# Optimization experiments

Hardware: AMD Instinct MI355X
Metric: run time of the kernel (lower is better)

## Reference

```python
import jax, jax.numpy as jnp
import numpy as np

N = 100000   # nodes
E = 1000000  # edges
IN, H, OUT = 256, 64, 16


def setup_inputs() -> dict:
    key = jax.random.key(0)
    k0, k1, k2, k3 = jax.random.split(key, 4)
    x = jax.random.normal(k0, (N, IN), jnp.float32)
    edge_index = jax.random.randint(k1, (2, E), 0, N)
    # GCNConv parameters (glorot-ish weights, zero bias as in PyG defaults)
    W1 = jax.random.normal(k2, (IN, H), jnp.float32) / np.sqrt(IN).astype(np.float32)
    b1 = jnp.zeros((H,), jnp.float32)
    W2 = jax.random.normal(k3, (H, OUT), jnp.float32) / np.sqrt(H).astype(np.float32)
    b2 = jnp.zeros((OUT,), jnp.float32)
    return {"x": x, "edge_index": edge_index, "W1": W1, "b1": b1, "W2": W2, "b2": b2}


def gcn_conv(x, W, b, src, dst, n):
    # PyG GCNConv: h = x @ W; out[v] = sum_{(u->v)} norm(u,v) * h[u] + b
    h = x @ W                                    # [n, out]
    deg = jnp.zeros((n,), h.dtype).at[dst].add(1.0)
    dinv = jnp.where(deg > 0, jax.lax.rsqrt(deg), 0.0)
    norm = dinv[src] * dinv[dst]                 # [E+n] symmetric normalization
    msg = h[src] * norm[:, None]                 # gather + scale
    agg = jax.ops.segment_sum(msg, dst, num_segments=n)  # scatter-add
    return agg + b


def reference(x, edge_index, W1, b1, W2, b2):
    n = x.shape[0]
    # add self-loops (PyG GCNConv default add_self_loops=True)
    loops = jnp.arange(n, dtype=edge_index.dtype)
    src = jnp.concatenate([edge_index[0], loops])
    dst = jnp.concatenate([edge_index[1], loops])
    h = gcn_conv(x, W1, b1, src, dst, n)
    h = jax.nn.relu(h)  # F.dropout is identity in eval mode (training=False)
    return gcn_conv(h, W2, b2, src, dst, n)
```

## Files before the change

### kernel.cpp

```cpp
#include <hip/hip_runtime.h>

namespace {
constexpr int NN  = 100000;
constexpr int NE  = 1000000;
constexpr int INF = 256;
constexpr int HF  = 64;
constexpr int OF  = 16;
constexpr int SCAN_CHUNK = 1024;
constexpr int NBLK = (NN + SCAN_CHUNK - 1) / SCAN_CHUNK;
constexpr int NSEG = 8;
constexpr int SEGW = (NN + NSEG - 1) / NSEG;
constexpr int CNTW = 100096;
constexpr int ZBLK = (CNTW / 4 + 255) / 256;
constexpr int GB   = (NN + 127) / 128;
constexpr int ECHUNK = 2048;
constexpr int EGRP = (NE + ECHUNK - 1) / ECHUNK;
constexpr int SB   = EGRP * NSEG;
}

typedef __attribute__((ext_vector_type(8))) short     sh8;
typedef __attribute__((ext_vector_type(4))) float     f32x4;
typedef __attribute__((ext_vector_type(8))) unsigned short us8;

__device__ __forceinline__ unsigned short f2bf(float f) {
    unsigned int u = __builtin_bit_cast(unsigned int, f);
    u += 0x7FFFu + ((u >> 16) & 1u);
    return (unsigned short)(u >> 16);
}
__device__ __forceinline__ float bf2f(unsigned short s) {
    return __builtin_bit_cast(float, (unsigned int)s << 16);
}

__global__ void k_pre(int* __restrict__ cnt, const float* __restrict__ W1,
                      unsigned short* __restrict__ wt_g) {
    int b = blockIdx.x, t = threadIdx.x;
    if (b < ZBLK) {
        int i = (b * 256 + t) * 4;
        if (i < CNTW) *(int4*)(cnt + i) = (int4){0, 0, 0, 0};
    } else {
        int idx = (b - ZBLK) * 256 + t;
        int c = idx >> 8, k = idx & 255;
        wt_g[idx] = f2bf(W1[(size_t)k * HF + c]);
    }
}

__global__ __launch_bounds__(256) void k_hist(const int* __restrict__ dst,
                                              int* __restrict__ cnt) {
    int b   = blockIdx.x;
    int seg = b & (NSEG - 1);
    int grp = b >> 3;
    int e0  = grp * ECHUNK + threadIdx.x;
    int d[8];
    #pragma unroll
    for (int i = 0; i < 8; ++i) {
        int e = e0 + i * 256;
        d[i] = (e < NE) ? dst[e] : -1;
    }
    #pragma unroll
    for (int i = 0; i < 8; ++i) {
        if ((unsigned)d[i] / (unsigned)SEGW == (unsigned)seg)
            atomicAdd(&cnt[d[i]], 1);
    }
}

__global__ __launch_bounds__(256) void k_reduce(const int* __restrict__ cnt,
                                                int* __restrict__ bsum,
                                                float* __restrict__ dinv) {
    int t = threadIdx.x;
    int i0 = blockIdx.x * SCAN_CHUNK + t * 4;
    int s = 0;
    float dv[4] = {0.f, 0.f, 0.f, 0.f};
    #pragma unroll
    for (int q = 0; q < 4; ++q) {
        if (i0 + q < NN) {
            int c = cnt[i0 + q];
            s += c;
            dv[q] = rsqrtf((float)(c + 1));
        }
    }
    if (i0 + 3 < NN) *(float4*)(dinv + i0) = (float4){dv[0], dv[1], dv[2], dv[3]};
    else { for (int q = 0; q < 4; ++q) if (i0 + q < NN) dinv[i0 + q] = dv[q]; }
    #pragma unroll
    for (int off = 32; off > 0; off >>= 1) s += __shfl_down(s, off);
    __shared__ int wsum[4];
    int lane = t & 63, wid = t >> 6;
    if (lane == 0) wsum[wid] = s;
    __syncthreads();
    if (t == 0) bsum[blockIdx.x] = wsum[0] + wsum[1] + wsum[2] + wsum[3];
}

__global__ __launch_bounds__(256) void k_scan(const int* __restrict__ cnt,
                                              const int* __restrict__ bsum,
                                              int* __restrict__ rowptr,
                                              int* __restrict__ cursor) {
    int t = threadIdx.x;
    int b = blockIdx.x;
    int lane = t & 63, wid = t >> 6;

    int p = 0;
    if (lane < b) p += bsum[lane];
    if (64 + lane < b) p += bsum[64 + lane];
    #pragma unroll
    for (int off = 32; off > 0; off >>= 1) p += __shfl_down(p, off);
    int blockBase = __shfl(p, 0);

    int i0 = b * SCAN_CHUNK + t * 4;
    int v0 = 0, v1 = 0, v2 = 0, v3 = 0;
    if (i0 + 0 < NN) v0 = cnt[i0 + 0];
    if (i0 + 1 < NN) v1 = cnt[i0 + 1];
    if (i0 + 2 < NN) v2 = cnt[i0 + 2];
    if (i0 + 3 < NN) v3 = cnt[i0 + 3];
    int tsum = v0 + v1 + v2 + v3;
    int incl = tsum;
    #pragma unroll
    for (int off = 1; off < 64; off <<= 1) {
        int n = __shfl_up(incl, off);
        if (lane >= off) incl += n;
    }
    __shared__ int wsum[4];
    if (lane == 63) wsum[wid] = incl;
    __syncthreads();
    int woff = 0;
    for (int w = 0; w < wid; ++w) woff += wsum[w];
    int excl = woff + (incl - tsum) + blockBase;
    int e0 = excl, e1 = e0 + v0, e2 = e1 + v1, e3 = e2 + v2;
    if (i0 + 0 < NN) { rowptr[i0 + 0] = e0; cursor[i0 + 0] = e0; }
    if (i0 + 1 < NN) { rowptr[i0 + 1] = e1; cursor[i0 + 1] = e1; }
    if (i0 + 2 < NN) { rowptr[i0 + 2] = e2; cursor[i0 + 2] = e2; }
    if (i0 + 3 < NN) { rowptr[i0 + 3] = e3; cursor[i0 + 3] = e3; }
    if (i0 + 3 == NN - 1) rowptr[NN] = e3 + v3;
}

__global__ __launch_bounds__(256, 8) void k_gs(const float* __restrict__ x,
                                               const unsigned short* __restrict__ wt_g,
                                               unsigned short* __restrict__ h1,
                                               const int* __restrict__ src,
                                               const int* __restrict__ dst,
                                               int* __restrict__ cursor,
                                               int* __restrict__ eidx) {
    __shared__ unsigned short wt[64 * 136];
    int b = blockIdx.x;
    int t = threadIdx.x;

    if (b >= GB) {
        int sb  = b - GB;
        int seg = sb & (NSEG - 1);
        int grp = sb >> 3;
        int e0  = grp * ECHUNK + t;
        int d[8];
        #pragma unroll
        for (int i = 0; i < 8; ++i) {
            int e = e0 + i * 256;
            d[i] = (e < NE) ? dst[e] : -1;
        }
        #pragma unroll
        for (int i = 0; i < 8; ++i) {
            if ((unsigned)d[i] / (unsigned)SEGW == (unsigned)seg) {
                int p = atomicAdd(&cursor[d[i]], 1);
                eidx[p] = src[e0 + i * 256];
            }
        }
        return;
    }

    int w = t >> 6, l = t & 63;
    int row0 = b * 128;
    int m = l & 15;
    int g = l >> 4;
    int gr0 = row0 + w * 32 + m;      if (gr0 > NN - 1) gr0 = NN - 1;
    int gr1 = row0 + w * 32 + 16 + m; if (gr1 > NN - 1) gr1 = NN - 1;
    const float* p0 = x + (size_t)gr0 * INF + g * 8;
    const float* p1 = x + (size_t)gr1 * INF + g * 8;

    f32x4 acc[2][4];
    #pragma unroll
    for (int i = 0; i < 2; ++i)
        #pragma unroll
        for (int j = 0; j < 4; ++j) acc[i][j] = (f32x4){0.f, 0.f, 0.f, 0.f};

    #pragma unroll
    for (int half = 0; half < 2; ++half) {
        __syncthreads();
        #pragma unroll
        for (int p = 0; p < 4; ++p) {
            int T   = p * 256 + t;
            int c   = T >> 4;
            int kb8 = T & 15;
            *(us8*)(wt + c * 136 + kb8 * 8) =
                *(const us8*)(wt_g + c * 256 + half * 128 + kb8 * 8);
        }
        __syncthreads();

        #pragma unroll
        for (int kb = 0; kb < 128; kb += 32) {
            float4 u0 = *(const float4*)(p0 + half * 128 + kb);
            float4 u1 = *(const float4*)(p0 + half * 128 + kb + 4);
            float4 u2 = *(const float4*)(p1 + half * 128 + kb);
            float4 u3 = *(const float4*)(p1 + half * 128 + kb + 4);
            us8 a0u = { f2bf(u0.x), f2bf(u0.y), f2bf(u0.z), f2bf(u0.w),
                        f2bf(u1.x), f2bf(u1.y), f2bf(u1.z), f2bf(u1.w) };
            us8 a1u = { f2bf(u2.x), f2bf(u2.y), f2bf(u2.z), f2bf(u2.w),
                        f2bf(u3.x), f2bf(u3.y), f2bf(u3.z), f2bf(u3.w) };
            sh8 a0 = __builtin_bit_cast(sh8, a0u);
            sh8 a1 = __builtin_bit_cast(sh8, a1u);
            #pragma unroll
            for (int nt = 0; nt < 4; ++nt) {
                sh8 bb = *(const sh8*)(wt + (nt * 16 + m) * 136 + kb + g * 8);
                acc[0][nt] = __builtin_amdgcn_mfma_f32_16x16x32_bf16(a0, bb, acc[0][nt], 0, 0, 0);
                acc[1][nt] = __builtin_amdgcn_mfma_f32_16x16x32_bf16(a1, bb, acc[1][nt], 0, 0, 0);
            }
        }
    }

    #pragma unroll
    for (int mt = 0; mt < 2; ++mt) {
        #pragma unroll
        for (int r = 0; r < 4; ++r) {
            int gr = row0 + w * 32 + mt * 16 + (l >> 4) * 4 + r;
            if (gr < NN) {
                #pragma unroll
                for (int nt = 0; nt < 4; ++nt)
                    h1[(size_t)gr * HF + nt * 16 + (l & 15)] = f2bf(acc[mt][nt][r]);
            }
        }
    }
}

__global__ __launch_bounds__(256) void k_gather1(const int* __restrict__ rowptr,
                                                 const int* __restrict__ eidx,
                                                 const float* __restrict__ dinv,
                                                 const unsigned short* __restrict__ h1,
                                                 const float* __restrict__ b1,
                                                 const float* __restrict__ W2,
                                                 unsigned short* __restrict__ h2) {
    __shared__ float w2L[HF * OF];
    __shared__ float hrL[32][HF + 4];
    int t = threadIdx.x;
    *(float4*)(w2L + t * 4) = *(const float4*)(W2 + t * 4);

    int nodeL = t >> 3;
    int fg    = t & 7;
    int v     = blockIdx.x * 32 + nodeL;
    int beg = rowptr[v], end = rowptr[v + 1];

    float acc[8] = {};
    int   s_n = 0;  float w_n = 0.f;  us8 h_n = {};
    if (beg < end) {
        s_n = eidx[beg];
        w_n = dinv[s_n];
        h_n = *(const us8*)(h1 + (size_t)s_n * HF + fg * 8);
    }
    for (int i = beg; i < end; ++i) {
        float w_c = w_n;  us8 h_c = h_n;
        if (i + 1 < end) {
            s_n = eidx[i + 1];
            w_n = dinv[s_n];
            h_n = *(const us8*)(h1 + (size_t)s_n * HF + fg * 8);
        }
        #pragma unroll
        for (int q = 0; q < 8; ++q) acc[q] += w_c * bf2f(h_c[q]);
    }

    {
        float dv = dinv[v], sl = dv * dv;
        us8 hv = *(const us8*)(h1 + (size_t)v * HF + fg * 8);
        #pragma unroll
        for (int q = 0; q < 8; ++q) {
            float val = dv * acc[q] + sl * bf2f(hv[q]) + b1[fg * 8 + q];
            hrL[nodeL][fg * 8 + q] = val > 0.f ? val : 0.f;
        }
    }
    __syncthreads();

    #pragma unroll
    for (int T = t; T < 512; T += 256) {
        int n = T >> 4, j = T & 15;
        const float* hr = hrL[n];
        float p = 0.f;
        #pragma unroll
        for (int k = 0; k < HF; ++k) p += hr[k] * w2L[k * OF + j];
        h2[(size_t)(blockIdx.x * 32 + n) * OF + j] = f2bf(p);
    }
}

__global__ __launch_bounds__(256) void k_gather2(const int* __restrict__ rowptr,
                                                 const int* __restrict__ eidx,
                                                 const float* __restrict__ dinv,
                                                 const unsigned short* __restrict__ h2,
                                                 const float* __restrict__ b2,
                                                 float* __restrict__ out) {
    int t     = threadIdx.x;
    int nodeL = t >> 4;
    int j     = t & 15;
    int v     = blockIdx.x * 16 + nodeL;
    int beg = rowptr[v], end = rowptr[v + 1];

    float acc = 0.f;
    int   s_n = 0;  float w_n = 0.f;  unsigned short h_n = 0;
    if (beg < end) {
        s_n = eidx[beg];
        w_n = dinv[s_n];
        h_n = h2[(size_t)s_n * OF + j];
    }
    for (int i = beg; i < end; ++i) {
        float w_c = w_n;  unsigned short h_c = h_n;
        if (i + 1 < end) {
            s_n = eidx[i + 1];
            w_n = dinv[s_n];
            h_n = h2[(size_t)s_n * OF + j];
        }
        acc += w_c * bf2f(h_c);
    }
    float dv = dinv[v];
    out[(size_t)v * OF + j] = dv * acc + dv * dv * bf2f(h2[(size_t)v * OF + j]) + b2[j];
}

extern "C" void kernel_launch(void* const* d_in, const int* in_sizes, int n_in,
                              void* d_out, int out_size, void* d_ws, size_t ws_size,
                              hipStream_t stream) {
    const float* x   = (const float*)d_in[0];
    const int*   ei  = (const int*)d_in[1];
    const int*   src = ei;
    const int*   dst = ei + NE;
    const float* W1  = (const float*)d_in[2];
    const float* b1  = (const float*)d_in[3];
    const float* W2  = (const float*)d_in[4];
    const float* b2  = (const float*)d_in[5];
    float* out = (float*)d_out;

    float* dinv  = (float*)d_ws;
    unsigned short* h1b = (unsigned short*)(dinv + CNTW);
    unsigned short* h2b = (unsigned short*)(h1b + (size_t)NN * HF);
    int*   cnt   = (int*)(h2b + (size_t)NN * OF + (size_t)NN * OF);
    int*   rowptr = cnt + CNTW;
    int*   cursor = rowptr + 100352;
    int*   eidx  = cursor + CNTW;
    int*   bsum  = eidx + NE;
    unsigned short* wt_g = (unsigned short*)(bsum + 128);

    k_pre<<<ZBLK + 64, 256, 0, stream>>>(cnt, W1, wt_g);
    k_hist<<<SB, 256, 0, stream>>>(dst, cnt);
    k_reduce<<<NBLK, 256, 0, stream>>>(cnt, bsum, dinv);
    k_scan<<<NBLK, 256, 0, stream>>>(cnt, bsum, rowptr, cursor);

    k_gs<<<GB + SB, 256, 0, stream>>>(x, wt_g, h1b, src, dst, cursor, eidx);

    k_gather1<<<NN / 32, 256, 0, stream>>>(rowptr, eidx, dinv, h1b, b1, W2, h2b);

    k_gather2<<<NN / 16, 256, 0, stream>>>(rowptr, eidx, dinv, h2b, b2, out);
}
```

Before: 180.3 us.

## Split GEMM1 across histogram and scatter kernels to overlap with atomics

The first-layer GEMM (x@W1) is split into two halves. One half runs in the same launch as the degree histogram and the other half in the same launch as the CSR scatter. Previously the histogram ran alone and the whole GEMM shared a launch with the scatter. This balances compute-heavy GEMM blocks against atomic-bound edge blocks in both launches, so latency-bound atomics overlap with bandwidth-bound GEMM work. The GEMM body becomes a shared device function, and the shared-memory footprint now also applies to the histogram blocks.

```diff
diff --git a/kernel.cpp b/kernel.cpp
--- a/kernel.cpp
+++ b/kernel.cpp
@@ -13,6 +13,8 @@
 constexpr int CNTW = 100096;
 constexpr int ZBLK = (CNTW / 4 + 255) / 256;
 constexpr int GB   = (NN + 127) / 128;
+constexpr int GBH  = GB / 2;
+constexpr int GBR  = GB - GBH;
 constexpr int ECHUNK = 2048;
 constexpr int EGRP = (NE + ECHUNK - 1) / ECHUNK;
 constexpr int SB   = EGRP * NSEG;
@@ -44,127 +46,13 @@
     }
 }
 
-__global__ __launch_bounds__(256) void k_hist(const int* __restrict__ dst,
-                                              int* __restrict__ cnt) {
-    int b   = blockIdx.x;
-    int seg = b & (NSEG - 1);
-    int grp = b >> 3;
-    int e0  = grp * ECHUNK + threadIdx.x;
-    int d[8];
-    #pragma unroll
-    for (int i = 0; i < 8; ++i) {
-        int e = e0 + i * 256;
-        d[i] = (e < NE) ? dst[e] : -1;
-    }
-    #pragma unroll
-    for (int i = 0; i < 8; ++i) {
-        if ((unsigned)d[i] / (unsigned)SEGW == (unsigned)seg)
-            atomicAdd(&cnt[d[i]], 1);
-    }
-}
-
-__global__ __launch_bounds__(256) void k_reduce(const int* __restrict__ cnt,
-                                                int* __restrict__ bsum,
-                                                float* __restrict__ dinv) {
-    int t = threadIdx.x;
-    int i0 = blockIdx.x * SCAN_CHUNK + t * 4;
-    int s = 0;
-    float dv[4] = {0.f, 0.f, 0.f, 0.f};
-    #pragma unroll
-    for (int q = 0; q < 4; ++q) {
-        if (i0 + q < NN) {
-            int c = cnt[i0 + q];
-            s += c;
-            dv[q] = rsqrtf((float)(c + 1));
-        }
-    }
-    if (i0 + 3 < NN) *(float4*)(dinv + i0) = (float4){dv[0], dv[1], dv[2], dv[3]};
-    else { for (int q = 0; q < 4; ++q) if (i0 + q < NN) dinv[i0 + q] = dv[q]; }
-    #pragma unroll
-    for (int off = 32; off > 0; off >>= 1) s += __shfl_down(s, off);
-    __shared__ int wsum[4];
-    int lane = t & 63, wid = t >> 6;
-    if (lane == 0) wsum[wid] = s;
-    __syncthreads();
-    if (t == 0) bsum[blockIdx.x] = wsum[0] + wsum[1] + wsum[2] + wsum[3];
-}
-
-__global__ __launch_bounds__(256) void k_scan(const int* __restrict__ cnt,
-                                              const int* __restrict__ bsum,
-                                              int* __restrict__ rowptr,
-                                              int* __restrict__ cursor) {
-    int t = threadIdx.x;
-    int b = blockIdx.x;
-    int lane = t & 63, wid = t >> 6;
-
-    int p = 0;
-    if (lane < b) p += bsum[lane];
-    if (64 + lane < b) p += bsum[64 + lane];
-    #pragma unroll
-    for (int off = 32; off > 0; off >>= 1) p += __shfl_down(p, off);
-    int blockBase = __shfl(p, 0);
-
-    int i0 = b * SCAN_CHUNK + t * 4;
-    int v0 = 0, v1 = 0, v2 = 0, v3 = 0;
-    if (i0 + 0 < NN) v0 = cnt[i0 + 0];
-    if (i0 + 1 < NN) v1 = cnt[i0 + 1];
-    if (i0 + 2 < NN) v2 = cnt[i0 + 2];
-    if (i0 + 3 < NN) v3 = cnt[i0 + 3];
-    int tsum = v0 + v1 + v2 + v3;
-    int incl = tsum;
-    #pragma unroll
-    for (int off = 1; off < 64; off <<= 1) {
-        int n = __shfl_up(incl, off);
-        if (lane >= off) incl += n;
-    }
-    __shared__ int wsum[4];
-    if (lane == 63) wsum[wid] = incl;
-    __syncthreads();
-    int woff = 0;
-    for (int w = 0; w < wid; ++w) woff += wsum[w];
-    int excl = woff + (incl - tsum) + blockBase;
-    int e0 = excl, e1 = e0 + v0, e2 = e1 + v1, e3 = e2 + v2;
-    if (i0 + 0 < NN) { rowptr[i0 + 0] = e0; cursor[i0 + 0] = e0; }
-    if (i0 + 1 < NN) { rowptr[i0 + 1] = e1; cursor[i0 + 1] = e1; }
-    if (i0 + 2 < NN) { rowptr[i0 + 2] = e2; cursor[i0 + 2] = e2; }
-    if (i0 + 3 < NN) { rowptr[i0 + 3] = e3; cursor[i0 + 3] = e3; }
-    if (i0 + 3 == NN - 1) rowptr[NN] = e3 + v3;
-}
-
-__global__ __launch_bounds__(256, 8) void k_gs(const float* __restrict__ x,
-                                               const unsigned short* __restrict__ wt_g,
-                                               unsigned short* __restrict__ h1,
-                                               const int* __restrict__ src,
-                                               const int* __restrict__ dst,
-                                               int* __restrict__ cursor,
-                                               int* __restrict__ eidx) {
-    __shared__ unsigned short wt[64 * 136];
-    int b = blockIdx.x;
-    int t = threadIdx.x;
-
-    if (b >= GB) {
-        int sb  = b - GB;
-        int seg = sb & (NSEG - 1);
-        int grp = sb >> 3;
-        int e0  = grp * ECHUNK + t;
-        int d[8];
-        #pragma unroll
-        for (int i = 0; i < 8; ++i) {
-            int e = e0 + i * 256;
-            d[i] = (e < NE) ? dst[e] : -1;
-        }
-        #pragma unroll
-        for (int i = 0; i < 8; ++i) {
-            if ((unsigned)d[i] / (unsigned)SEGW == (unsigned)seg) {
-                int p = atomicAdd(&cursor[d[i]], 1);
-                eidx[p] = src[e0 + i * 256];
-            }
-        }
-        return;
-    }
-
+__device__ __forceinline__ void gemm1_block(int gb, int t,
+                                            const float* __restrict__ x,
+                                            const unsigned short* __restrict__ wt_g,
+                                            unsigned short* __restrict__ h1,
+                                            unsigned short* wt ) {
     int w = t >> 6, l = t & 63;
-    int row0 = b * 128;
+    int row0 = gb * 128;
     int m = l & 15;
     int g = l >> 4;
     int gr0 = row0 + w * 32 + m;      if (gr0 > NN - 1) gr0 = NN - 1;
@@ -226,6 +114,138 @@
     }
 }
 
+__global__ __launch_bounds__(256, 8) void k_gh(const float* __restrict__ x,
+                                               const unsigned short* __restrict__ wt_g,
+                                               unsigned short* __restrict__ h1,
+                                               const int* __restrict__ dst,
+                                               int* __restrict__ cnt) {
+    __shared__ unsigned short wt[64 * 136];
+    int b = blockIdx.x;
+    int t = threadIdx.x;
+
+    if (b >= GBH) {
+        int hb  = b - GBH;
+        int seg = hb & (NSEG - 1);
+        int grp = hb >> 3;
+        int e0  = grp * ECHUNK + t;
+        int d[8];
+        #pragma unroll
+        for (int i = 0; i < 8; ++i) {
+            int e = e0 + i * 256;
+            d[i] = (e < NE) ? dst[e] : -1;
+        }
+        #pragma unroll
+        for (int i = 0; i < 8; ++i) {
+            if ((unsigned)d[i] / (unsigned)SEGW == (unsigned)seg)
+                atomicAdd(&cnt[d[i]], 1);
+        }
+        return;
+    }
+    gemm1_block(b, t, x, wt_g, h1, wt);
+}
+
+__global__ __launch_bounds__(256, 8) void k_gsc(const float* __restrict__ x,
+                                                const unsigned short* __restrict__ wt_g,
+                                                unsigned short* __restrict__ h1,
+                                                const int* __restrict__ src,
+                                                const int* __restrict__ dst,
+                                                int* __restrict__ cursor,
+                                                int* __restrict__ eidx) {
+    __shared__ unsigned short wt[64 * 136];
+    int b = blockIdx.x;
+    int t = threadIdx.x;
+
+    if (b >= GBR) {
+        int sb  = b - GBR;
+        int seg = sb & (NSEG - 1);
+        int grp = sb >> 3;
+        int e0  = grp * ECHUNK + t;
+        int d[8];
+        #pragma unroll
+        for (int i = 0; i < 8; ++i) {
+            int e = e0 + i * 256;
+            d[i] = (e < NE) ? dst[e] : -1;
+        }
+        #pragma unroll
+        for (int i = 0; i < 8; ++i) {
+            if ((unsigned)d[i] / (unsigned)SEGW == (unsigned)seg) {
+                int p = atomicAdd(&cursor[d[i]], 1);
+                eidx[p] = src[e0 + i * 256];
+            }
+        }
+        return;
+    }
+    gemm1_block(b + GBH, t, x, wt_g, h1, wt);
+}
+
+__global__ __launch_bounds__(256) void k_reduce(const int* __restrict__ cnt,
+                                                int* __restrict__ bsum,
+                                                float* __restrict__ dinv) {
+    int t = threadIdx.x;
+    int i0 = blockIdx.x * SCAN_CHUNK + t * 4;
+    int s = 0;
+    float dv[4] = {0.f, 0.f, 0.f, 0.f};
+    #pragma unroll
+    for (int q = 0; q < 4; ++q) {
+        if (i0 + q < NN) {
+            int c = cnt[i0 + q];
+            s += c;
+            dv[q] = rsqrtf((float)(c + 1));
+        }
+    }
+    if (i0 + 3 < NN) *(float4*)(dinv + i0) = (float4){dv[0], dv[1], dv[2], dv[3]};
+    else { for (int q = 0; q < 4; ++q) if (i0 + q < NN) dinv[i0 + q] = dv[q]; }
+    #pragma unroll
+    for (int off = 32; off > 0; off >>= 1) s += __shfl_down(s, off);
+    __shared__ int wsum[4];
+    int lane = t & 63, wid = t >> 6;
+    if (lane == 0) wsum[wid] = s;
+    __syncthreads();
+    if (t == 0) bsum[blockIdx.x] = wsum[0] + wsum[1] + wsum[2] + wsum[3];
+}
+
+__global__ __launch_bounds__(256) void k_scan(const int* __restrict__ cnt,
+                                              const int* __restrict__ bsum,
+                                              int* __restrict__ rowptr,
+                                              int* __restrict__ cursor) {
+    int t = threadIdx.x;
+    int b = blockIdx.x;
+    int lane = t & 63, wid = t >> 6;
+
+    int p = 0;
+    if (lane < b) p += bsum[lane];
+    if (64 + lane < b) p += bsum[64 + lane];
+    #pragma unroll
+    for (int off = 32; off > 0; off >>= 1) p += __shfl_down(p, off);
+    int blockBase = __shfl(p, 0);
+
+    int i0 = b * SCAN_CHUNK + t * 4;
+    int v0 = 0, v1 = 0, v2 = 0, v3 = 0;
+    if (i0 + 0 < NN) v0 = cnt[i0 + 0];
+    if (i0 + 1 < NN) v1 = cnt[i0 + 1];
+    if (i0 + 2 < NN) v2 = cnt[i0 + 2];
+    if (i0 + 3 < NN) v3 = cnt[i0 + 3];
+    int tsum = v0 + v1 + v2 + v3;
+    int incl = tsum;
+    #pragma unroll
+    for (int off = 1; off < 64; off <<= 1) {
+        int n = __shfl_up(incl, off);
+        if (lane >= off) incl += n;
+    }
+    __shared__ int wsum[4];
+    if (lane == 63) wsum[wid] = incl;
+    __syncthreads();
+    int woff = 0;
+    for (int w = 0; w < wid; ++w) woff += wsum[w];
+    int excl = woff + (incl - tsum) + blockBase;
+    int e0 = excl, e1 = e0 + v0, e2 = e1 + v1, e3 = e2 + v2;
+    if (i0 + 0 < NN) { rowptr[i0 + 0] = e0; cursor[i0 + 0] = e0; }
+    if (i0 + 1 < NN) { rowptr[i0 + 1] = e1; cursor[i0 + 1] = e1; }
+    if (i0 + 2 < NN) { rowptr[i0 + 2] = e2; cursor[i0 + 2] = e2; }
+    if (i0 + 3 < NN) { rowptr[i0 + 3] = e3; cursor[i0 + 3] = e3; }
+    if (i0 + 3 == NN - 1) rowptr[NN] = e3 + v3;
+}
+
 __global__ __launch_bounds__(256) void k_gather1(const int* __restrict__ rowptr,
                                                  const int* __restrict__ eidx,
                                                  const float* __restrict__ dinv,
@@ -339,11 +359,12 @@
     unsigned short* wt_g = (unsigned short*)(bsum + 128);
 
     k_pre<<<ZBLK + 64, 256, 0, stream>>>(cnt, W1, wt_g);
-    k_hist<<<SB, 256, 0, stream>>>(dst, cnt);
+    k_gh<<<GBH + SB, 256, 0, stream>>>(x, wt_g, h1b, dst, cnt);
+
     k_reduce<<<NBLK, 256, 0, stream>>>(cnt, bsum, dinv);
     k_scan<<<NBLK, 256, 0, stream>>>(cnt, bsum, rowptr, cursor);
 
-    k_gs<<<GB + SB, 256, 0, stream>>>(x, wt_g, h1b, src, dst, cursor, eidx);
+    k_gsc<<<GBR + SB, 256, 0, stream>>>(x, wt_g, h1b, src, dst, cursor, eidx);
 
     k_gather1<<<NN / 32, 256, 0, stream>>>(rowptr, eidx, dinv, h1b, b1, W2, h2b);
 
```

Result: slower. 184.8 us (+2.5%).
